# Kernel optimization log

Measured on AMD Instinct MI355X. Metric: run time of the kernel, lower is better.

## Reference

```python
import jax, jax.numpy as jnp
import numpy as np

ALPHA = 2.0          # spikingjelly surrogate.ATan default alpha
V_THRESHOLD = 1.0    # IFNode default
# v_reset = 0.0 -> hard reset

@jax.custom_vjp
def atan_spike(x):
    # Heaviside forward, ATan surrogate backward
    return (x >= 0).astype(x.dtype)

def _atan_fwd(x):
    return atan_spike(x), x

def _atan_bwd(x, g):
    sg = (ALPHA / 2.0) / (1.0 + (jnp.pi / 2.0 * ALPHA * x) ** 2)
    return (g * sg,)

atan_spike.defvjp(_atan_fwd, _atan_bwd)

def if_node(x_seq):
    # x_seq: [T, B, D]; IF neuron: v += x; spike = H(v - th); hard reset to 0.
    # detach_reset=True -> stop_gradient on spike in the reset path.
    def step(v, xt):
        v = v + xt
        s = atan_spike(v - V_THRESHOLD)
        v = v * (1.0 - jax.lax.stop_gradient(s))
        return v, s
    v0 = jnp.zeros(x_seq.shape[1:], x_seq.dtype)
    _, spikes = jax.lax.scan(step, v0, x_seq)
    return spikes

def setup_inputs() -> dict:
    key = jax.random.key(0)
    k0, k1, k2, k3, k4 = jax.random.split(key, 5)
    B = 65536
    x = jax.random.normal(k0, (B, 1, 28, 28), dtype=jnp.float32)
    # Linear(28, 32) and Linear(32, 10) params (PyTorch layout: [out, in])
    W1 = jax.random.uniform(k1, (32, 28), jnp.float32, -1.0, 1.0) / np.sqrt(28.0).astype(np.float32)
    b1 = jax.random.uniform(k2, (32,), jnp.float32, -1.0, 1.0) / np.sqrt(28.0).astype(np.float32)
    W2 = jax.random.uniform(k3, (10, 32), jnp.float32, -1.0, 1.0) / np.sqrt(32.0).astype(np.float32)
    b2 = jax.random.uniform(k4, (10,), jnp.float32, -1.0, 1.0) / np.sqrt(32.0).astype(np.float32)
    return {"x": x, "W1": W1, "b1": b1, "W2": W2, "b2": b2}

def reference(x, W1, b1, W2, b2):
    # x: [B, 1, 28, 28] -> squeeze(1) -> [B, 28, 28] -> permute(2,0,1) -> [T=28, B, 28]
    xs = jnp.transpose(x[:, 0], (2, 0, 1))
    h1 = jnp.einsum('tbi,oi->tbo', xs, W1) + b1   # [28, B, 32]
    s1 = if_node(h1)
    h2 = jnp.einsum('tbi,oi->tbo', s1, W2) + b2   # [28, B, 10]
    s2 = if_node(h2)
    return s2.mean(axis=0)                         # [B, 10] firing rates
```

## Files before the change

### kernel.cpp

```cpp
#include <hip/hip_runtime.h>


#define THREADS 256
#define GRID    768
#define SPB     16

__global__ __launch_bounds__(THREADS, 3) void snn_if_kernel(
    const float* __restrict__ x,
    const float* __restrict__ W1,
    const float* __restrict__ b1,
    const float* __restrict__ W2,
    const float* __restrict__ b2,
    float* __restrict__ out,
    int B, int nIter)
{
    __shared__ float Ws[32 * 29];
    __shared__ float T4[1280];
    __shared__ float P[10240];

    const int tid = threadIdx.x;
    const int p   = tid & 15;
    const int g16 = (tid & 63) >> 4;
    const int sl  = tid >> 4;

    for (int e = tid; e < 32 * 28; e += THREADS) {
        int o = e / 28, i = e - o * 28;
        Ws[o * 29 + i] = W1[e];
    }
    for (int e = tid; e < 1280; e += THREADS) {
        int o2 = e % 10;
        int tn = e / 10;
        int nb = tn & 15, k = tn >> 4;
        float v = 0.f;
        if (nb & 1) v += W2[o2 * 32 + 4 * k + 0];
        if (nb & 2) v += W2[o2 * 32 + 4 * k + 1];
        if (nb & 4) v += W2[o2 * 32 + 4 * k + 2];
        if (nb & 8) v += W2[o2 * 32 + 4 * k + 3];
        T4[e] = v;
    }
    __syncthreads();
    for (int e = tid; e < 10240; e += THREADS) {
        int o2 = e % 10;
        int r  = e / 10;
        int bb = r & 255, g = r >> 8;
        P[e] = T4[((2 * g    ) * 16 + (bb & 15)) * 10 + o2]
             + T4[((2 * g + 1) * 16 + (bb >> 4)) * 10 + o2];
    }

    const float b1a = b1[p];
    const float b1b = b1[p + 16];
    const float b2o = (p < 10) ? b2[p] : 0.f;
    __syncthreads();

    for (int it = 0; it < nIter; ++it) {
        int samp = (blockIdx.x * nIter + it) * SPB + sl;
        bool ok  = (samp < B);
        const float* xs = x + (size_t)(ok ? samp : 0) * 784;

        float accA[28], accB[28];
        #pragma unroll
        for (int t = 0; t < 28; ++t) { accA[t] = 0.f; accB[t] = 0.f; }

        float4 c[7], n[7];
        {
            const float4* r0 = (const float4*)xs;
            #pragma unroll
            for (int q = 0; q < 7; ++q) c[q] = r0[q];
        }

        #pragma unroll 1
        for (int i = 0; i < 28; i += 2) {
            const float4* rn = (const float4*)(xs + (i + 1) * 28);
            #pragma unroll
            for (int q = 0; q < 7; ++q) n[q] = rn[q];
            float wA = Ws[p * 29 + i];
            float wB = Ws[(p + 16) * 29 + i];
            #pragma unroll
            for (int q = 0; q < 7; ++q) {
                accA[4*q+0] = fmaf(wA, c[q].x, accA[4*q+0]);
                accA[4*q+1] = fmaf(wA, c[q].y, accA[4*q+1]);
                accA[4*q+2] = fmaf(wA, c[q].z, accA[4*q+2]);
                accA[4*q+3] = fmaf(wA, c[q].w, accA[4*q+3]);
                accB[4*q+0] = fmaf(wB, c[q].x, accB[4*q+0]);
                accB[4*q+1] = fmaf(wB, c[q].y, accB[4*q+1]);
                accB[4*q+2] = fmaf(wB, c[q].z, accB[4*q+2]);
                accB[4*q+3] = fmaf(wB, c[q].w, accB[4*q+3]);
            }
            const float4* rc = (const float4*)(xs + (i + 2 < 28 ? i + 2 : 0) * 28);
            #pragma unroll
            for (int q = 0; q < 7; ++q) c[q] = rc[q];
            float wA1 = Ws[p * 29 + i + 1];
            float wB1 = Ws[(p + 16) * 29 + i + 1];
            #pragma unroll
            for (int q = 0; q < 7; ++q) {
                accA[4*q+0] = fmaf(wA1, n[q].x, accA[4*q+0]);
                accA[4*q+1] = fmaf(wA1, n[q].y, accA[4*q+1]);
                accA[4*q+2] = fmaf(wA1, n[q].z, accA[4*q+2]);
                accA[4*q+3] = fmaf(wA1, n[q].w, accA[4*q+3]);
                accB[4*q+0] = fmaf(wB1, n[q].x, accB[4*q+0]);
                accB[4*q+1] = fmaf(wB1, n[q].y, accB[4*q+1]);
                accB[4*q+2] = fmaf(wB1, n[q].z, accB[4*q+2]);
                accB[4*q+3] = fmaf(wB1, n[q].w, accB[4*q+3]);
            }
        }

        float v1a = 0.f, v1b = 0.f, v2 = 0.f, cnt = 0.f;
        #pragma unroll
        for (int t = 0; t < 28; ++t) {
            v1a += accA[t] + b1a;
            v1b += accB[t] + b1b;
            bool sA = (v1a >= 1.0f);
            bool sB = (v1b >= 1.0f);
            unsigned long long balA = __ballot(sA);
            unsigned long long balB = __ballot(sB);
            if (sA) v1a = 0.f;
            if (sB) v1b = 0.f;
            unsigned mlo = (unsigned)(balA >> (g16 * 16)) & 0xFFFFu;
            unsigned mhi = (unsigned)(balB >> (g16 * 16)) & 0xFFFFu;
            unsigned m = mlo | (mhi << 16);

            if (p < 10) {
                unsigned c0 =  m        & 255u;
                unsigned c1 = (m >> 8)  & 255u;
                unsigned c2 = (m >> 16) & 255u;
                unsigned c3 =  m >> 24;
                float a2 =  P[(        c0) * 10 + p];
                a2      +=  P[( 256u + c1) * 10 + p];
                a2      +=  P[( 512u + c2) * 10 + p];
                a2      +=  P[( 768u + c3) * 10 + p];
                v2 += a2 + b2o;
                if (v2 >= 1.0f) { cnt += 1.f; v2 = 0.f; }
            }
        }

        if (p < 10 && ok) {
            out[(size_t)samp * 10 + p] = cnt / 28.0f;
        }
    }
}

extern "C" void kernel_launch(void* const* d_in, const int* in_sizes, int n_in,
                              void* d_out, int out_size, void* d_ws, size_t ws_size,
                              hipStream_t stream) {
    const float* x  = (const float*)d_in[0];
    const float* W1 = (const float*)d_in[1];
    const float* b1 = (const float*)d_in[2];
    const float* W2 = (const float*)d_in[3];
    const float* b2 = (const float*)d_in[4];
    float* out = (float*)d_out;

    int B = in_sizes[0] / 784;
    int nIter = (B + GRID * SPB - 1) / (GRID * SPB);
    snn_if_kernel<<<GRID, THREADS, 0, stream>>>(x, W1, b1, W2, b2, out, B, nIter);
}
```

Measured before the change: 410.0 us.

## Drop 40KB byte lookup table, use nibble table, one block per 16 samples

Removes the 256-entry-per-byte precomputed layer-2 table (40KB LDS) and instead sums eight lookups into the smaller 4-bit nibble table. This cuts LDS per block so more blocks fit per CU, and launch bounds rise from 3 to 6. The persistent grid-stride loop is replaced by one block per 16 samples (4096 blocks). The trade-off is twice as many LDS reads per timestep in the second layer, plus repeated table setup in every block. The tighter launch bound may also force register spills given the 56 accumulators.

```diff
diff --git a/kernel.cpp b/kernel.cpp
--- a/kernel.cpp
+++ b/kernel.cpp
@@ -2,21 +2,19 @@
 
 
 #define THREADS 256
-#define GRID    768
 #define SPB     16
 
-__global__ __launch_bounds__(THREADS, 3) void snn_if_kernel(
+__global__ __launch_bounds__(THREADS, 6) void snn_if_kernel(
     const float* __restrict__ x,
     const float* __restrict__ W1,
     const float* __restrict__ b1,
     const float* __restrict__ W2,
     const float* __restrict__ b2,
     float* __restrict__ out,
-    int B, int nIter)
+    int B)
 {
     __shared__ float Ws[32 * 29];
     __shared__ float T4[1280];
-    __shared__ float P[10240];
 
     const int tid = threadIdx.x;
     const int p   = tid & 15;
@@ -38,104 +36,92 @@
         if (nb & 8) v += W2[o2 * 32 + 4 * k + 3];
         T4[e] = v;
     }
-    __syncthreads();
-    for (int e = tid; e < 10240; e += THREADS) {
-        int o2 = e % 10;
-        int r  = e / 10;
-        int bb = r & 255, g = r >> 8;
-        P[e] = T4[((2 * g    ) * 16 + (bb & 15)) * 10 + o2]
-             + T4[((2 * g + 1) * 16 + (bb >> 4)) * 10 + o2];
-    }
 
     const float b1a = b1[p];
     const float b1b = b1[p + 16];
     const float b2o = (p < 10) ? b2[p] : 0.f;
     __syncthreads();
 
-    for (int it = 0; it < nIter; ++it) {
-        int samp = (blockIdx.x * nIter + it) * SPB + sl;
-        bool ok  = (samp < B);
-        const float* xs = x + (size_t)(ok ? samp : 0) * 784;
+    int samp = blockIdx.x * SPB + sl;
+    bool ok  = (samp < B);
+    const float* xs = x + (size_t)(ok ? samp : 0) * 784;
 
-        float accA[28], accB[28];
+    float accA[28], accB[28];
+    #pragma unroll
+    for (int t = 0; t < 28; ++t) { accA[t] = 0.f; accB[t] = 0.f; }
+
+    float4 c[7], n[7];
+    {
+        const float4* r0 = (const float4*)xs;
         #pragma unroll
-        for (int t = 0; t < 28; ++t) { accA[t] = 0.f; accB[t] = 0.f; }
+        for (int q = 0; q < 7; ++q) c[q] = r0[q];
+    }
 
-        float4 c[7], n[7];
-        {
-            const float4* r0 = (const float4*)xs;
+    #pragma unroll 1
+    for (int i = 0; i < 28; i += 2) {
+        const float4* rn = (const float4*)(xs + (i + 1) * 28);
+        #pragma unroll
+        for (int q = 0; q < 7; ++q) n[q] = rn[q];
+        float wA = Ws[p * 29 + i];
+        float wB = Ws[(p + 16) * 29 + i];
+        #pragma unroll
+        for (int q = 0; q < 7; ++q) {
+            accA[4*q+0] = fmaf(wA, c[q].x, accA[4*q+0]);
+            accA[4*q+1] = fmaf(wA, c[q].y, accA[4*q+1]);
+            accA[4*q+2] = fmaf(wA, c[q].z, accA[4*q+2]);
+            accA[4*q+3] = fmaf(wA, c[q].w, accA[4*q+3]);
+            accB[4*q+0] = fmaf(wB, c[q].x, accB[4*q+0]);
+            accB[4*q+1] = fmaf(wB, c[q].y, accB[4*q+1]);
+            accB[4*q+2] = fmaf(wB, c[q].z, accB[4*q+2]);
+            accB[4*q+3] = fmaf(wB, c[q].w, accB[4*q+3]);
+        }
+        const float4* rc = (const float4*)(xs + (i + 2 < 28 ? i + 2 : 0) * 28);
+        #pragma unroll
+        for (int q = 0; q < 7; ++q) c[q] = rc[q];
+        float wA1 = Ws[p * 29 + i + 1];
+        float wB1 = Ws[(p + 16) * 29 + i + 1];
+        #pragma unroll
+        for (int q = 0; q < 7; ++q) {
+            accA[4*q+0] = fmaf(wA1, n[q].x, accA[4*q+0]);
+            accA[4*q+1] = fmaf(wA1, n[q].y, accA[4*q+1]);
+            accA[4*q+2] = fmaf(wA1, n[q].z, accA[4*q+2]);
+            accA[4*q+3] = fmaf(wA1, n[q].w, accA[4*q+3]);
+            accB[4*q+0] = fmaf(wB1, n[q].x, accB[4*q+0]);
+            accB[4*q+1] = fmaf(wB1, n[q].y, accB[4*q+1]);
+            accB[4*q+2] = fmaf(wB1, n[q].z, accB[4*q+2]);
+            accB[4*q+3] = fmaf(wB1, n[q].w, accB[4*q+3]);
+        }
+    }
+
+    float v1a = 0.f, v1b = 0.f, v2 = 0.f, cnt = 0.f;
+    #pragma unroll
+    for (int t = 0; t < 28; ++t) {
+        v1a += accA[t] + b1a;
+        v1b += accB[t] + b1b;
+        bool sA = (v1a >= 1.0f);
+        bool sB = (v1b >= 1.0f);
+        unsigned long long balA = __ballot(sA);
+        unsigned long long balB = __ballot(sB);
+        if (sA) v1a = 0.f;
+        if (sB) v1b = 0.f;
+        unsigned mlo = (unsigned)(balA >> (g16 * 16)) & 0xFFFFu;
+        unsigned mhi = (unsigned)(balB >> (g16 * 16)) & 0xFFFFu;
+        unsigned m = mlo | (mhi << 16);
+
+        if (p < 10) {
+            float a2 = 0.f;
             #pragma unroll
-            for (int q = 0; q < 7; ++q) c[q] = r0[q];
+            for (int k = 0; k < 8; ++k) {
+                unsigned nib = (m >> (4 * k)) & 15u;
+                a2 += T4[k * 160 + nib * 10 + p];
+            }
+            v2 += a2 + b2o;
+            if (v2 >= 1.0f) { cnt += 1.f; v2 = 0.f; }
         }
+    }
 
-        #pragma unroll 1
-        for (int i = 0; i < 28; i += 2) {
-            const float4* rn = (const float4*)(xs + (i + 1) * 28);
-            #pragma unroll
-            for (int q = 0; q < 7; ++q) n[q] = rn[q];
-            float wA = Ws[p * 29 + i];
-            float wB = Ws[(p + 16) * 29 + i];
-            #pragma unroll
-            for (int q = 0; q < 7; ++q) {
-                accA[4*q+0] = fmaf(wA, c[q].x, accA[4*q+0]);
-                accA[4*q+1] = fmaf(wA, c[q].y, accA[4*q+1]);
-                accA[4*q+2] = fmaf(wA, c[q].z, accA[4*q+2]);
-                accA[4*q+3] = fmaf(wA, c[q].w, accA[4*q+3]);
-                accB[4*q+0] = fmaf(wB, c[q].x, accB[4*q+0]);
-                accB[4*q+1] = fmaf(wB, c[q].y, accB[4*q+1]);
-                accB[4*q+2] = fmaf(wB, c[q].z, accB[4*q+2]);
-                accB[4*q+3] = fmaf(wB, c[q].w, accB[4*q+3]);
-            }
-            const float4* rc = (const float4*)(xs + (i + 2 < 28 ? i + 2 : 0) * 28);
-            #pragma unroll
-            for (int q = 0; q < 7; ++q) c[q] = rc[q];
-            float wA1 = Ws[p * 29 + i + 1];
-            float wB1 = Ws[(p + 16) * 29 + i + 1];
-            #pragma unroll
-            for (int q = 0; q < 7; ++q) {
-                accA[4*q+0] = fmaf(wA1, n[q].x, accA[4*q+0]);
-                accA[4*q+1] = fmaf(wA1, n[q].y, accA[4*q+1]);
-                accA[4*q+2] = fmaf(wA1, n[q].z, accA[4*q+2]);
-                accA[4*q+3] = fmaf(wA1, n[q].w, accA[4*q+3]);
-                accB[4*q+0] = fmaf(wB1, n[q].x, accB[4*q+0]);
-                accB[4*q+1] = fmaf(wB1, n[q].y, accB[4*q+1]);
-                accB[4*q+2] = fmaf(wB1, n[q].z, accB[4*q+2]);
-                accB[4*q+3] = fmaf(wB1, n[q].w, accB[4*q+3]);
-            }
-        }
-
-        float v1a = 0.f, v1b = 0.f, v2 = 0.f, cnt = 0.f;
-        #pragma unroll
-        for (int t = 0; t < 28; ++t) {
-            v1a += accA[t] + b1a;
-            v1b += accB[t] + b1b;
-            bool sA = (v1a >= 1.0f);
-            bool sB = (v1b >= 1.0f);
-            unsigned long long balA = __ballot(sA);
-            unsigned long long balB = __ballot(sB);
-            if (sA) v1a = 0.f;
-            if (sB) v1b = 0.f;
-            unsigned mlo = (unsigned)(balA >> (g16 * 16)) & 0xFFFFu;
-            unsigned mhi = (unsigned)(balB >> (g16 * 16)) & 0xFFFFu;
-            unsigned m = mlo | (mhi << 16);
-
-            if (p < 10) {
-                unsigned c0 =  m        & 255u;
-                unsigned c1 = (m >> 8)  & 255u;
-                unsigned c2 = (m >> 16) & 255u;
-                unsigned c3 =  m >> 24;
-                float a2 =  P[(        c0) * 10 + p];
-                a2      +=  P[( 256u + c1) * 10 + p];
-                a2      +=  P[( 512u + c2) * 10 + p];
-                a2      +=  P[( 768u + c3) * 10 + p];
-                v2 += a2 + b2o;
-                if (v2 >= 1.0f) { cnt += 1.f; v2 = 0.f; }
-            }
-        }
-
-        if (p < 10 && ok) {
-            out[(size_t)samp * 10 + p] = cnt / 28.0f;
-        }
+    if (p < 10 && ok) {
+        out[(size_t)samp * 10 + p] = cnt / 28.0f;
     }
 }
 
@@ -150,6 +136,6 @@
     float* out = (float*)d_out;
 
     int B = in_sizes[0] / 784;
-    int nIter = (B + GRID * SPB - 1) / (GRID * SPB);
-    snn_if_kernel<<<GRID, THREADS, 0, stream>>>(x, W1, b1, W2, b2, out, B, nIter);
+    int grid = (B + SPB - 1) / SPB;
+    snn_if_kernel<<<grid, THREADS, 0, stream>>>(x, W1, b1, W2, b2, out, B);
 }
```

Result: slower. 510.6 us (+24.5%).
